# Performance work log

Hardware: AMD Instinct MI355X
Metric: run time of the kernel (lower is better)

## Reference

```python
import jax, jax.numpy as jnp
import numpy as np

D_MODEL = 512
N_HEADS = 8
HEAD_DIM = D_MODEL // N_HEADS  # 64


def setup_inputs() -> dict:
    key = jax.random.key(0)
    ks = jax.random.split(key, 12)
    B, SQ, SK = 4, 2048, 2048
    s = 1.0 / np.sqrt(D_MODEL)
    return {
        "query": jax.random.normal(ks[0], (B, SQ, D_MODEL), jnp.float32),
        "key": jax.random.normal(ks[1], (B, SK, D_MODEL), jnp.float32),
        "value": jax.random.normal(ks[2], (B, SK, D_MODEL), jnp.float32),
        "Wq": jax.random.normal(ks[3], (D_MODEL, D_MODEL), jnp.float32) * s,
        "bq": jnp.zeros((D_MODEL,), jnp.float32),
        "Wk": jax.random.normal(ks[4], (D_MODEL, D_MODEL), jnp.float32) * s,
        "bk": jnp.zeros((D_MODEL,), jnp.float32),
        "Wv": jax.random.normal(ks[5], (D_MODEL, D_MODEL), jnp.float32) * s,
        "bv": jnp.zeros((D_MODEL,), jnp.float32),
        "Wo": jax.random.normal(ks[6], (D_MODEL, D_MODEL), jnp.float32) * s,
        "bo": jnp.zeros((D_MODEL,), jnp.float32),
    }


def reference(query, key, value, Wq, bq, Wk, bk, Wv, bv, Wo, bo):
    B, SQ, _ = query.shape
    SK = key.shape[1]
    # QKV projections
    Q = query @ Wq.T + bq  # [B,SQ,D]
    K = key @ Wk.T + bk    # [B,SK,D]
    V = value @ Wv.T + bv  # [B,SK,D]
    # split heads -> [B,H,S,hd]
    Q = Q.reshape(B, SQ, N_HEADS, HEAD_DIM).transpose(0, 2, 1, 3)
    K = K.reshape(B, SK, N_HEADS, HEAD_DIM).transpose(0, 2, 1, 3)
    V = V.reshape(B, SK, N_HEADS, HEAD_DIM).transpose(0, 2, 1, 3)
    scale = jnp.sqrt(jnp.float32(HEAD_DIM))
    scores = jnp.einsum('bhqd,bhkd->bhqk', Q, K) / scale  # [B,H,SQ,SK]
    attn = jax.nn.softmax(scores, axis=-1)  # dropout p=0 (eval)
    ctx = jnp.einsum('bhqk,bhkd->bhqd', attn, V)
    ctx = ctx.transpose(0, 2, 1, 3).reshape(B, SQ, D_MODEL)
    # exact (erf) GELU as in torch F.gelu default
    out = jax.nn.gelu(ctx, approximate=False) @ Wo.T + bo
    return out
```

## Files before the change

### kernel.cpp

```cpp
#include <hip/hip_runtime.h>
#include <hip/hip_bf16.h>

#define D_MODEL 512
#define N_HEADS 8
#define HEAD_DIM 64
#define BATCH 4
#define SEQ 2048

typedef _Float16 f16;
typedef _Float16 f16x8 __attribute__((ext_vector_type(8)));
typedef _Float16 f16x4 __attribute__((ext_vector_type(4)));
typedef float f32x4 __attribute__((ext_vector_type(4)));
typedef unsigned int u32x4 __attribute__((ext_vector_type(4)));

#define MFMA16(a, b, c) __builtin_amdgcn_mfma_f32_16x16x32_f16((a), (b), (c), 0, 0, 0)

#define GLOAD_LDS16(src, dst)                                                   \
    __builtin_amdgcn_global_load_lds(                                           \
        (const __attribute__((address_space(1))) void*)(src),                   \
        (__attribute__((address_space(3))) void*)(dst), 16, 0, 0)

#if __has_builtin(__builtin_amdgcn_exp2f)
#define EXP2(x) __builtin_amdgcn_exp2f(x)
#else
#define EXP2(x) __expf((x) * 0.6931471805599453f)
#endif

#define QSCALE 0.18033688011112042f
#define OFF2 8.656170245333781f

__global__ __launch_bounds__(256) void wsplit(
    const float* __restrict__ w0, const float* __restrict__ w1,
    const float* __restrict__ w2, const float* __restrict__ w3,
    f16* __restrict__ h0, f16* __restrict__ h1,
    f16* __restrict__ h2, f16* __restrict__ h3)
{
    const int j = blockIdx.y;
    const float* s = (j == 0) ? w0 : (j == 1) ? w1 : (j == 2) ? w2 : w3;
    f16* dh = (j == 0) ? h0 : (j == 1) ? h1 : (j == 2) ? h2 : h3;
    const int n4 = (D_MODEL * D_MODEL) >> 2;
    for (int i = blockIdx.x * 256 + threadIdx.x; i < n4; i += gridDim.x * 256) {
        float4 x = ((const float4*)s)[i];
        f16x4 hv = {(f16)x.x, (f16)x.y, (f16)x.z, (f16)x.w};
        ((f16x4*)dh)[i] = hv;
    }
}

__global__ __launch_bounds__(512, 4) void proj_mfma(
    const float* __restrict__ Xq, const float* __restrict__ Xk,
    const float* __restrict__ Xv,
    const f16* __restrict__ Wqh, const f16* __restrict__ Wkh,
    const f16* __restrict__ Wvh,
    const float* __restrict__ bq, const float* __restrict__ bk,
    const float* __restrict__ bv,
    f16* __restrict__ Qh, f16* __restrict__ Kh, f16* __restrict__ Vt)
{
    __shared__ f16 ldsA[128 * 64];
    __shared__ f16 ldsW[256 * 64];

    const int z = blockIdx.z;
    const float* X = (z == 0) ? Xq : (z == 1) ? Xk : Xv;
    const f16* Wh = (z == 0) ? Wqh : (z == 1) ? Wkh : Wvh;
    const float* bias = (z == 0) ? bq : (z == 1) ? bk : bv;

    const int m0 = blockIdx.x * 128;
    const int n0 = blockIdx.y * 256;

    const int tid = threadIdx.x;
    const int w = tid >> 6, l = tid & 63;
    const int lp = l >> 4, lq = l & 15;
    const int wm = w >> 2, wn = w & 3;

    f32x4 acc[4][4] = {};

    for (int kt = 0; kt < D_MODEL; kt += 64) {
        __syncthreads();
        float4 av[2][2];
        int arow[2], aslot[2];
#pragma unroll
        for (int j = 0; j < 2; ++j) {
            const int chunk = j * 512 + tid;
            arow[j] = chunk >> 3;
            aslot[j] = chunk & 7;
            const float* sp = X + (size_t)(m0 + arow[j]) * D_MODEL + kt + aslot[j] * 8;
            av[j][0] = *(const float4*)sp;
            av[j][1] = *(const float4*)(sp + 4);
        }
#pragma unroll
        for (int j = 0; j < 4; ++j) {
            const int cb = j * 512 + w * 64;
            const int chunk = cb + l;
            const int row = chunk >> 3;
            const int slot = (chunk & 7) ^ (row & 7);
            GLOAD_LDS16(Wh + (size_t)(n0 + row) * D_MODEL + kt + slot * 8,
                        ldsW + cb * 8);
        }
#pragma unroll
        for (int j = 0; j < 2; ++j) {
            f16x8 hv;
            hv[0] = (f16)av[j][0].x; hv[1] = (f16)av[j][0].y;
            hv[2] = (f16)av[j][0].z; hv[3] = (f16)av[j][0].w;
            hv[4] = (f16)av[j][1].x; hv[5] = (f16)av[j][1].y;
            hv[6] = (f16)av[j][1].z; hv[7] = (f16)av[j][1].w;
            *(f16x8*)(ldsA + arow[j] * 64 + ((aslot[j] ^ (arow[j] & 7)) << 3)) = hv;
        }
        __syncthreads();

        f16x8 af[4][2];
#pragma unroll
        for (int mt = 0; mt < 4; ++mt) {
            const int R = wm * 64 + mt * 16 + lq;
#pragma unroll
            for (int s = 0; s < 2; ++s)
                af[mt][s] = *(const f16x8*)(ldsA + R * 64 + (((s * 4 + lp) ^ (R & 7)) << 3));
        }
        __builtin_amdgcn_s_setprio(1);
#pragma unroll
        for (int nt = 0; nt < 4; ++nt) {
            const int R = wn * 64 + nt * 16 + lq;
            f16x8 b0 = *(const f16x8*)(ldsW + R * 64 + (((0 + lp) ^ (R & 7)) << 3));
            f16x8 b1 = *(const f16x8*)(ldsW + R * 64 + (((4 + lp) ^ (R & 7)) << 3));
#pragma unroll
            for (int mt = 0; mt < 4; ++mt) {
                acc[mt][nt] = MFMA16(af[mt][0], b0, acc[mt][nt]);
                acc[mt][nt] = MFMA16(af[mt][1], b1, acc[mt][nt]);
            }
        }
        __builtin_amdgcn_s_setprio(0);
    }

    const int m_base = m0 + wm * 64;
    const int n_base = n0 + wn * 64;
    const int b = m0 / SEQ;
    const int h = n_base >> 6;
    const size_t bh_ = (size_t)b * N_HEADS + h;

    if (z == 0) {
#pragma unroll
        for (int nt = 0; nt < 4; ++nt) {
            const int n = n_base + nt * 16 + lq;
            const float bn = bias[n];
            const int d = n & 63;
#pragma unroll
            for (int mt = 0; mt < 4; ++mt) {
#pragma unroll
                for (int r = 0; r < 4; ++r) {
                    const int s = (m_base + mt * 16 + lp * 4 + r) & (SEQ - 1);
                    Qh[(bh_ * SEQ + s) * 64 + d] = (f16)((acc[mt][nt][r] + bn) * QSCALE);
                }
            }
        }
    } else if (z == 1) {
#pragma unroll
        for (int nt = 0; nt < 4; ++nt) {
            const int n = n_base + nt * 16 + lq;
            const float bn = bias[n];
            const int d = n & 63;
#pragma unroll
            for (int mt = 0; mt < 4; ++mt) {
#pragma unroll
                for (int r = 0; r < 4; ++r) {
                    const int s = (m_base + mt * 16 + lp * 4 + r) & (SEQ - 1);
                    Kh[(bh_ * SEQ + s) * 64 + d] = (f16)(acc[mt][nt][r] + bn);
                }
            }
        }
    } else {
#pragma unroll
        for (int nt = 0; nt < 4; ++nt) {
            const int n = n_base + nt * 16 + lq;
            const float bn = bias[n];
            const int d = n & 63;
#pragma unroll
            for (int mt = 0; mt < 4; ++mt) {
                const int s0 = (m_base + mt * 16 + lp * 4) & (SEQ - 1);
                f16x4 col;
#pragma unroll
                for (int r = 0; r < 4; ++r)
                    col[r] = (f16)(acc[mt][nt][r] + bn);
                *(f16x4*)(Vt + (bh_ * 64 + d) * SEQ + s0) = col;
            }
        }
    }
}

__global__ __launch_bounds__(256, 4) void out_mfma(
    const f16* __restrict__ Gh, const f16* __restrict__ Woh,
    const float* __restrict__ bo, float* __restrict__ Out)
{
    __shared__ f16 ldsA[64 * 64];
    __shared__ f16 ldsW[128 * 64];

    const int m0 = blockIdx.x * 64;
    const int n0 = blockIdx.y * 128;

    const int tid = threadIdx.x;
    const int w = tid >> 6, l = tid & 63;
    const int lp = l >> 4, lq = l & 15;
    const int wm = w >> 1, wn = w & 1;

    f32x4 acc[2][4] = {};

    for (int kt = 0; kt < D_MODEL; kt += 64) {
        __syncthreads();
#pragma unroll
        for (int j = 0; j < 2; ++j) {
            const int cb = j * 256 + w * 64;
            const int chunk = cb + l;
            const int row = chunk >> 3;
            const int slot = (chunk & 7) ^ (row & 7);
            GLOAD_LDS16(Gh + (size_t)(m0 + row) * D_MODEL + kt + slot * 8,
                        ldsA + cb * 8);
        }
#pragma unroll
        for (int j = 0; j < 4; ++j) {
            const int cb = j * 256 + w * 64;
            const int chunk = cb + l;
            const int row = chunk >> 3;
            const int slot = (chunk & 7) ^ (row & 7);
            GLOAD_LDS16(Woh + (size_t)(n0 + row) * D_MODEL + kt + slot * 8,
                        ldsW + cb * 8);
        }
        __syncthreads();

        f16x8 af[2][2];
#pragma unroll
        for (int mt = 0; mt < 2; ++mt) {
            const int R = wm * 32 + mt * 16 + lq;
#pragma unroll
            for (int s = 0; s < 2; ++s)
                af[mt][s] = *(const f16x8*)(ldsA + R * 64 + (((s * 4 + lp) ^ (R & 7)) << 3));
        }
        __builtin_amdgcn_s_setprio(1);
#pragma unroll
        for (int nt = 0; nt < 4; ++nt) {
            const int R = wn * 64 + nt * 16 + lq;
            f16x8 b0 = *(const f16x8*)(ldsW + R * 64 + (((0 + lp) ^ (R & 7)) << 3));
            f16x8 b1 = *(const f16x8*)(ldsW + R * 64 + (((4 + lp) ^ (R & 7)) << 3));
#pragma unroll
            for (int mt = 0; mt < 2; ++mt) {
                acc[mt][nt] = MFMA16(af[mt][0], b0, acc[mt][nt]);
                acc[mt][nt] = MFMA16(af[mt][1], b1, acc[mt][nt]);
            }
        }
        __builtin_amdgcn_s_setprio(0);
    }

#pragma unroll
    for (int nt = 0; nt < 4; ++nt) {
        const int n = n0 + wn * 64 + nt * 16 + lq;
        const float bn = bo[n];
#pragma unroll
        for (int mt = 0; mt < 2; ++mt) {
#pragma unroll
            for (int r = 0; r < 4; ++r) {
                const int m = m0 + wm * 32 + mt * 16 + lp * 4 + r;
                Out[(size_t)m * D_MODEL + n] = acc[mt][nt][r] + bn;
            }
        }
    }
}

__global__ __launch_bounds__(256, 2) void flash_mfma(
    const f16* __restrict__ Qh, const f16* __restrict__ Kh,
    const f16* __restrict__ Vt, f16* __restrict__ Gh)
{
    __shared__ f16 KV[2][2][4096];

    const int tid = threadIdx.x;
    const int w  = tid >> 6;
    const int l  = tid & 63;
    const int lp = l >> 4;
    const int lq = l & 15;

    const int id = blockIdx.x;
    const int work = (id & 7) * 64 + (id >> 3);
    const int bh = work >> 4;
    const int b  = bh >> 3, h = bh & 7;
    const int q0 = (work & 15) * 128 + w * 32;

    f16x8 qf[2][2];
#pragma unroll
    for (int sub = 0; sub < 2; ++sub)
#pragma unroll
        for (int s = 0; s < 2; ++s)
            qf[sub][s] = *(const f16x8*)(Qh + ((size_t)bh * SEQ + q0 + sub * 16 + lq) * 64
                                          + s * 32 + lp * 8);

    f16x8 ones;
#pragma unroll
    for (int i = 0; i < 8; ++i) ones[i] = (f16)1.f;
    const f32x4 OFFI = (f32x4){-OFF2, -OFF2, -OFF2, -OFF2};

    f32x4 o[2][4];
#pragma unroll
    for (int sub = 0; sub < 2; ++sub)
#pragma unroll
        for (int c = 0; c < 4; ++c) o[sub][c] = (f32x4){0.f, 0.f, 0.f, 0.f};
    f32x4 lf[2] = {(f32x4){0.f, 0.f, 0.f, 0.f}, (f32x4){0.f, 0.f, 0.f, 0.f}};

    int koff[4][2], voff[2][4];
#pragma unroll
    for (int mt = 0; mt < 4; ++mt) {
        const int krow = mt * 16 + lq;
#pragma unroll
        for (int s = 0; s < 2; ++s)
            koff[mt][s] = krow * 128 + (((4 * s + lp) ^ (krow & 7)) << 4);
    }
#pragma unroll
    for (int s = 0; s < 2; ++s)
#pragma unroll
        for (int nt = 0; nt < 4; ++nt) {
            const int d = nt * 16 + lq;
            voff[s][nt] = d * 128 + (((4 * s + lp) ^ (d & 7)) << 4);
        }

    const int lr0 = w * 8 + (l >> 3);
    const int lr1 = (w + 4) * 8 + (l >> 3);
    const f16* kp0 = Kh + ((size_t)bh * SEQ + lr0) * 64 + (((l & 7) ^ (lr0 & 7)) << 3);
    const f16* kp1 = Kh + ((size_t)bh * SEQ + lr1) * 64 + (((l & 7) ^ (lr1 & 7)) << 3);
    const f16* vp0 = Vt + ((size_t)bh * 64 + lr0) * SEQ + (((l & 7) ^ (lr0 & 7)) << 3);
    const f16* vp1 = Vt + ((size_t)bh * 64 + lr1) * SEQ + (((l & 7) ^ (lr1 & 7)) << 3);

    auto STAGE = [&](int bf) {
        GLOAD_LDS16(kp0, &KV[bf][0][w * 512]);
        GLOAD_LDS16(kp1, &KV[bf][0][(w + 4) * 512]);
        GLOAD_LDS16(vp0, &KV[bf][1][w * 512]);
        GLOAD_LDS16(vp1, &KV[bf][1][(w + 4) * 512]);
        kp0 += 64 * 64; kp1 += 64 * 64;
        vp0 += 64;      vp1 += 64;
    };

    auto QKT = [&](int bf, f32x4 (&st)[2][4], f16x8 (&vbr)[2][4]) {
        const char* Kt_ = (const char*)&KV[bf][0][0];
        const char* Vt_ = (const char*)&KV[bf][1][0];
        __builtin_amdgcn_s_setprio(1);
#pragma unroll
        for (int mt = 0; mt < 4; ++mt) {
            f16x8 ah0 = *(const f16x8*)(Kt_ + koff[mt][0]);
            f16x8 ah1 = *(const f16x8*)(Kt_ + koff[mt][1]);
#pragma unroll
            for (int sub = 0; sub < 2; ++sub) {
                st[sub][mt] = MFMA16(ah0, qf[sub][0], OFFI);
                st[sub][mt] = MFMA16(ah1, qf[sub][1], st[sub][mt]);
            }
        }
        __builtin_amdgcn_s_setprio(0);
#pragma unroll
        for (int s = 0; s < 2; ++s)
#pragma unroll
            for (int nt = 0; nt < 4; ++nt)
                vbr[s][nt] = *(const f16x8*)(Vt_ + voff[s][nt]);
    };

    auto SMPV = [&](f32x4 (&st)[2][4], f16x8 (&vbr)[2][4]) {
        f16x8 pa[2][2];
#pragma unroll
        for (int sub = 0; sub < 2; ++sub) {
            unsigned int pk0[4], pk1[4];
#pragma unroll
            for (int mt = 0; mt < 4; ++mt) {
                float e0 = EXP2(st[sub][mt][0]);
                float e1 = EXP2(st[sub][mt][1]);
                float e2 = EXP2(st[sub][mt][2]);
                float e3 = EXP2(st[sub][mt][3]);
                pk0[mt] = __builtin_bit_cast(unsigned int,
                              __builtin_amdgcn_cvt_pkrtz(e0, e1));
                pk1[mt] = __builtin_bit_cast(unsigned int,
                              __builtin_amdgcn_cvt_pkrtz(e2, e3));
            }
#pragma unroll
            for (int s = 0; s < 2; ++s) {
                unsigned int x0 = pk0[2 * s], y0 = pk0[2 * s + 1];
                unsigned int x1 = pk1[2 * s], y1 = pk1[2 * s + 1];
                asm("v_permlane32_swap_b32 %0, %1" : "+v"(x0), "+v"(y0));
                asm("v_permlane16_swap_b32 %0, %1" : "+v"(x0), "+v"(y0));
                asm("v_permlane32_swap_b32 %0, %1" : "+v"(x1), "+v"(y1));
                asm("v_permlane16_swap_b32 %0, %1" : "+v"(x1), "+v"(y1));
                u32x4 t4 = {x0, x1, y0, y1};
                pa[sub][s] = __builtin_bit_cast(f16x8, t4);
            }
        }
        __builtin_amdgcn_s_setprio(1);
#pragma unroll
        for (int s = 0; s < 2; ++s) {
#pragma unroll
            for (int sub = 0; sub < 2; ++sub) {
                lf[sub] = MFMA16(pa[sub][s], ones, lf[sub]);
#pragma unroll
                for (int nt = 0; nt < 4; ++nt)
                    o[sub][nt] = MFMA16(pa[sub][s], vbr[s][nt], o[sub][nt]);
            }
        }
        __builtin_amdgcn_s_setprio(0);
    };

    f32x4 stA[2][4], stB[2][4];
    f16x8 vbrA[2][4], vbrB[2][4];

    STAGE(0);
    asm volatile("s_waitcnt vmcnt(0)" ::: "memory");
    __builtin_amdgcn_s_barrier();
    STAGE(1);
    __builtin_amdgcn_sched_barrier(0);
    QKT(0, stA, vbrA);

#pragma unroll 1
    for (int tt = 0; tt < 15; ++tt) {
        asm volatile("s_waitcnt vmcnt(0)" ::: "memory");
        __builtin_amdgcn_s_barrier();
        STAGE(0);
        __builtin_amdgcn_sched_barrier(0);
        QKT(1, stB, vbrB);
        SMPV(stA, vbrA);

        asm volatile("s_waitcnt vmcnt(0)" ::: "memory");
        __builtin_amdgcn_s_barrier();
        STAGE(1);
        __builtin_amdgcn_sched_barrier(0);
        QKT(0, stA, vbrA);
        SMPV(stB, vbrB);
    }

    asm volatile("s_waitcnt vmcnt(0)" ::: "memory");
    __builtin_amdgcn_s_barrier();
    __builtin_amdgcn_sched_barrier(0);
    QKT(1, stB, vbrB);
    SMPV(stA, vbrA);
    SMPV(stB, vbrB);

#pragma unroll
    for (int sub = 0; sub < 2; ++sub) {
#pragma unroll
        for (int j = 0; j < 4; ++j) {
            const float inv = 1.f / lf[sub][j];
            const int row = q0 + sub * 16 + lp * 4 + j;
#pragma unroll
            for (int nt = 0; nt < 4; ++nt) {
                float x = o[sub][nt][j] * inv;
                float g = 0.5f * x * (1.f + erff(x * 0.70710678118654752f));
                Gh[((size_t)(b * SEQ + row)) * D_MODEL + h * 64 + nt * 16 + lq] = (f16)g;
            }
        }
    }
}

extern "C" void kernel_launch(void* const* d_in, const int* in_sizes, int n_in,
                              void* d_out, int out_size, void* d_ws, size_t ws_size,
                              hipStream_t stream)
{
    const float* query = (const float*)d_in[0];
    const float* key   = (const float*)d_in[1];
    const float* value = (const float*)d_in[2];
    const float* Wq = (const float*)d_in[3];
    const float* bq = (const float*)d_in[4];
    const float* Wk = (const float*)d_in[5];
    const float* bk = (const float*)d_in[6];
    const float* Wv = (const float*)d_in[7];
    const float* bv = (const float*)d_in[8];
    const float* Wo = (const float*)d_in[9];
    const float* bo = (const float*)d_in[10];

    char* ws = (char*)d_ws;
    const size_t MB = 1024 * 1024;
    const size_t KB = 1024;
    f16* Qh = (f16*)(ws + 0 * MB);
    f16* Kh = (f16*)(ws + 8 * MB);
    f16* Vt = (f16*)(ws + 16 * MB);
    f16* Gh = (f16*)(ws + 24 * MB);
    f16* Wqh = (f16*)(ws + 32 * MB);
    f16* Wkh = (f16*)(ws + 32 * MB + 512 * KB);
    f16* Wvh = (f16*)(ws + 33 * MB);
    f16* Woh = (f16*)(ws + 33 * MB + 512 * KB);

    wsplit<<<dim3(64, 4), 256, 0, stream>>>(Wq, Wk, Wv, Wo, Wqh, Wkh, Wvh, Woh);

    proj_mfma<<<dim3(BATCH * SEQ / 128, D_MODEL / 256, 3), 512, 0, stream>>>(
        query, key, value, Wqh, Wkh, Wvh, bq, bk, bv, Qh, Kh, Vt);

    flash_mfma<<<dim3(512), 256, 0, stream>>>(Qh, Kh, Vt, Gh);

    out_mfma<<<dim3(BATCH * SEQ / 64, D_MODEL / 128), 256, 0, stream>>>(
        Gh, Woh, bo, (float*)d_out);
}
```

Before: 92.25 us.

## Shrink projection tiles to 128x128 and stage flash K/V in pairs

The projection kernel moves from 512-thread blocks with 128x256 tiles to 256-thread blocks with 128x128 tiles. This halves LDS per block and doubles the grid, at the cost of reloading and reconverting the fp32 activations twice as often. The flash attention kernel now loads two 64-key K/V tiles per barrier into a 4-buffer LDS ring. That halves the number of waitcnt/barrier syncs but doubles LDS use to 64KB, which may reduce occupancy. Each pair's QK^T products are computed together before its softmax/PV step, which changes how much the two overlap.

```diff
diff --git a/kernel.cpp b/kernel.cpp
--- a/kernel.cpp
+++ b/kernel.cpp
@@ -46,7 +46,7 @@
     }
 }
 
-__global__ __launch_bounds__(512, 4) void proj_mfma(
+__global__ __launch_bounds__(256, 3) void proj_mfma(
     const float* __restrict__ Xq, const float* __restrict__ Xk,
     const float* __restrict__ Xv,
     const f16* __restrict__ Wqh, const f16* __restrict__ Wkh,
@@ -56,7 +56,7 @@
     f16* __restrict__ Qh, f16* __restrict__ Kh, f16* __restrict__ Vt)
 {
     __shared__ f16 ldsA[128 * 64];
-    __shared__ f16 ldsW[256 * 64];
+    __shared__ f16 ldsW[128 * 64];
 
     const int z = blockIdx.z;
     const float* X = (z == 0) ? Xq : (z == 1) ? Xk : Xv;
@@ -64,22 +64,22 @@
     const float* bias = (z == 0) ? bq : (z == 1) ? bk : bv;
 
     const int m0 = blockIdx.x * 128;
-    const int n0 = blockIdx.y * 256;
+    const int n0 = blockIdx.y * 128;
 
     const int tid = threadIdx.x;
     const int w = tid >> 6, l = tid & 63;
     const int lp = l >> 4, lq = l & 15;
-    const int wm = w >> 2, wn = w & 3;
+    const int wm = w >> 1, wn = w & 1;
 
     f32x4 acc[4][4] = {};
 
     for (int kt = 0; kt < D_MODEL; kt += 64) {
         __syncthreads();
-        float4 av[2][2];
-        int arow[2], aslot[2];
-#pragma unroll
-        for (int j = 0; j < 2; ++j) {
-            const int chunk = j * 512 + tid;
+        float4 av[4][2];
+        int arow[4], aslot[4];
+#pragma unroll
+        for (int j = 0; j < 4; ++j) {
+            const int chunk = j * 256 + tid;
             arow[j] = chunk >> 3;
             aslot[j] = chunk & 7;
             const float* sp = X + (size_t)(m0 + arow[j]) * D_MODEL + kt + aslot[j] * 8;
@@ -88,7 +88,7 @@
         }
 #pragma unroll
         for (int j = 0; j < 4; ++j) {
-            const int cb = j * 512 + w * 64;
+            const int cb = j * 256 + w * 64;
             const int chunk = cb + l;
             const int row = chunk >> 3;
             const int slot = (chunk & 7) ^ (row & 7);
@@ -96,7 +96,7 @@
                         ldsW + cb * 8);
         }
 #pragma unroll
-        for (int j = 0; j < 2; ++j) {
+        for (int j = 0; j < 4; ++j) {
             f16x8 hv;
             hv[0] = (f16)av[j][0].x; hv[1] = (f16)av[j][0].y;
             hv[2] = (f16)av[j][0].z; hv[3] = (f16)av[j][0].w;
@@ -265,7 +265,7 @@
     const f16* __restrict__ Qh, const f16* __restrict__ Kh,
     const f16* __restrict__ Vt, f16* __restrict__ Gh)
 {
-    __shared__ f16 KV[2][2][4096];
+    __shared__ f16 KV[4][2][4096];
 
     const int tid = threadIdx.x;
     const int w  = tid >> 6;
@@ -322,13 +322,21 @@
     const f16* vp0 = Vt + ((size_t)bh * 64 + lr0) * SEQ + (((l & 7) ^ (lr0 & 7)) << 3);
     const f16* vp1 = Vt + ((size_t)bh * 64 + lr1) * SEQ + (((l & 7) ^ (lr1 & 7)) << 3);
 
-    auto STAGE = [&](int bf) {
-        GLOAD_LDS16(kp0, &KV[bf][0][w * 512]);
-        GLOAD_LDS16(kp1, &KV[bf][0][(w + 4) * 512]);
-        GLOAD_LDS16(vp0, &KV[bf][1][w * 512]);
-        GLOAD_LDS16(vp1, &KV[bf][1][(w + 4) * 512]);
-        kp0 += 64 * 64; kp1 += 64 * 64;
-        vp0 += 64;      vp1 += 64;
+    auto STAGE_PAIR = [&](int pr) {
+        f16* KA = &KV[pr * 2][0][0];
+        f16* VA = &KV[pr * 2][1][0];
+        f16* KB = &KV[pr * 2 + 1][0][0];
+        f16* VB = &KV[pr * 2 + 1][1][0];
+        GLOAD_LDS16(kp0, KA + w * 512);
+        GLOAD_LDS16(kp1, KA + (w + 4) * 512);
+        GLOAD_LDS16(vp0, VA + w * 512);
+        GLOAD_LDS16(vp1, VA + (w + 4) * 512);
+        GLOAD_LDS16(kp0 + 4096, KB + w * 512);
+        GLOAD_LDS16(kp1 + 4096, KB + (w + 4) * 512);
+        GLOAD_LDS16(vp0 + 64, VB + w * 512);
+        GLOAD_LDS16(vp1 + 64, VB + (w + 4) * 512);
+        kp0 += 8192; kp1 += 8192;
+        vp0 += 128;  vp1 += 128;
     };
 
     auto QKT = [&](int bf, f32x4 (&st)[2][4], f16x8 (&vbr)[2][4]) {
@@ -395,39 +403,26 @@
         __builtin_amdgcn_s_setprio(0);
     };
 
-    f32x4 stA[2][4], stB[2][4];
-    f16x8 vbrA[2][4], vbrB[2][4];
-
-    STAGE(0);
-    asm volatile("s_waitcnt vmcnt(0)" ::: "memory");
-    __builtin_amdgcn_s_barrier();
-    STAGE(1);
-    __builtin_amdgcn_sched_barrier(0);
-    QKT(0, stA, vbrA);
+    f32x4 stE[2][4], stO[2][4];
+    f16x8 vbrE[2][4], vbrO[2][4];
+
+    STAGE_PAIR(0);
+    int pr = 0;
 
 #pragma unroll 1
-    for (int tt = 0; tt < 15; ++tt) {
+    for (int t = 0; t < 16; ++t) {
         asm volatile("s_waitcnt vmcnt(0)" ::: "memory");
         __builtin_amdgcn_s_barrier();
-        STAGE(0);
+        if (t < 15) STAGE_PAIR(pr ^ 1);
         __builtin_amdgcn_sched_barrier(0);
-        QKT(1, stB, vbrB);
-        SMPV(stA, vbrA);
-
-        asm volatile("s_waitcnt vmcnt(0)" ::: "memory");
-        __builtin_amdgcn_s_barrier();
-        STAGE(1);
-        __builtin_amdgcn_sched_barrier(0);
-        QKT(0, stA, vbrA);
-        SMPV(stB, vbrB);
-    }
-
-    asm volatile("s_waitcnt vmcnt(0)" ::: "memory");
-    __builtin_amdgcn_s_barrier();
-    __builtin_amdgcn_sched_barrier(0);
-    QKT(1, stB, vbrB);
-    SMPV(stA, vbrA);
-    SMPV(stB, vbrB);
+
+        QKT(pr * 2, stE, vbrE);
+        QKT(pr * 2 + 1, stO, vbrO);
+        SMPV(stE, vbrE);
+        SMPV(stO, vbrO);
+
+        pr ^= 1;
+    }
 
 #pragma unroll
     for (int sub = 0; sub < 2; ++sub) {
@@ -475,7 +470,7 @@
 
     wsplit<<<dim3(64, 4), 256, 0, stream>>>(Wq, Wk, Wv, Wo, Wqh, Wkh, Wvh, Woh);
 
-    proj_mfma<<<dim3(BATCH * SEQ / 128, D_MODEL / 256, 3), 512, 0, stream>>>(
+    proj_mfma<<<dim3(BATCH * SEQ / 128, D_MODEL / 128, 3), 256, 0, stream>>>(
         query, key, value, Wqh, Wkh, Wvh, bq, bk, bv, Qh, Kh, Vt);
 
     flash_mfma<<<dim3(512), 256, 0, stream>>>(Qh, Kh, Vt, Gh);
```

Result: faster. 84.58 us, median of 3 (-8.3%).
